# Performance work log

Measured on AMD Instinct MI355X. Metric: run time of the kernel, lower is better.

## Reference

```python
import math
import jax, jax.numpy as jnp
import numpy as np

_INIT_LOG_GAIN = math.log(5.0)
B, L, D = 4, 1024, 256


def setup_inputs() -> dict:
    key = jax.random.key(0)
    kq, kk = jax.random.split(key)
    q = jax.random.normal(kq, (B, L, D), dtype=jnp.float32)
    k = jax.random.normal(kk, (B, L, D), dtype=jnp.float32)
    P_prev = jnp.zeros((B, D, D), dtype=jnp.float32)
    log_gain = jnp.full((D,), _INIT_LOG_GAIN, dtype=jnp.float32)
    output_scale = jnp.ones((D,), dtype=jnp.float32)
    return {"q": q, "k": k, "P_prev": P_prev, "log_gain": log_gain,
            "output_scale": output_scale}


def reference(q, k, P_prev, log_gain, output_scale):
    """Sequential rank-1 projection-state update + normalized matvec + gated tanh.

    q, k: [B, L, D]; P_prev: [B, D, D]. Returns (q_out [B,L,D], P_final [B,D,D]).
    """
    gain = jnp.exp(log_gain)  # effective gain, [D]

    def step(P, qk_t):
        q_t, k_t = qk_t                                   # each [B, D]
        P = P + jnp.einsum('bi,bj->bij', k_t, k_t)        # rank-1 update
        fro = jnp.sqrt(jnp.sum(P * P, axis=(-2, -1), keepdims=True))
        P_norm = P / (fro + 1e-7)
        q_aligned = jnp.einsum('bij,bj->bi', P_norm, q_t)
        q_safe = jnp.tanh(gain * q_aligned) * output_scale
        return P, q_safe

    # scan over the L time axis
    P_final, outs = jax.lax.scan(step, P_prev,
                                 (jnp.swapaxes(q, 0, 1), jnp.swapaxes(k, 0, 1)))
    q_out = jnp.swapaxes(outs, 0, 1)  # [B, L, D]
    return q_out, P_final
```

## Files before the change

kernel.cpp:

```cpp
#include <hip/hip_runtime.h>
#include <math.h>


typedef __attribute__((ext_vector_type(8))) short bf16x8;
typedef __attribute__((ext_vector_type(4))) float f32x4;

__device__ __forceinline__ unsigned short f2bf(float x) {
    union { float f; unsigned u; } c; c.f = x;
    return (unsigned short)((c.u + (0x7fffu + ((c.u >> 16) & 1u))) >> 16);
}
__device__ __forceinline__ unsigned f2bf2(float a, float b) {
    union { float f; unsigned u; } ca, cb; ca.f = a; cb.f = b;
    unsigned ua = ca.u + (0x7fffu + ((ca.u >> 16) & 1u));
    unsigned ub = cb.u + (0x7fffu + ((cb.u >> 16) & 1u));
    return (ua >> 16) | (ub & 0xffff0000u);
}
__device__ __forceinline__ float bf2f(unsigned short h) {
    union { unsigned u; float f; } c; c.u = ((unsigned)h) << 16; return c.f;
}
__device__ __forceinline__ void gload16(const void* g, const void* l) {
    __builtin_amdgcn_global_load_lds(
        (const __attribute__((address_space(1))) unsigned int*)g,
        (__attribute__((address_space(3))) unsigned int*)l, 16, 0, 0);
}
__device__ __forceinline__ bf16x8 ldsfrag(const unsigned short* lds, int row0, int g0, int lane) {
    int r = row0 + (lane & 15);
    int g = g0 + (lane >> 4);
    return *(const bf16x8*)(lds + r * 64 + (((g ^ (r & 7)) & 7) << 3));
}
#define MFMA16(a, b, c) __builtin_amdgcn_mfma_f32_16x16x32_bf16(a, b, c, 0, 0, 0)

__global__ __launch_bounds__(256) void k_prep(
    const float* __restrict__ Q, const float* __restrict__ K,
    const float* __restrict__ Pprev,
    unsigned short* __restrict__ Qb, unsigned short* __restrict__ Kb,
    unsigned short* __restrict__ KThi, unsigned short* __restrict__ KTlo,
    float* __restrict__ basePart, int B_, int L, int D)
{
    __shared__ float lds[64 * 65];
    int tid = threadIdx.x, lane = tid & 63, w = tid >> 6;
    int nDt = D >> 6, nLt = L >> 6;
    int nC = B_ * nLt * nDt;
    int id = blockIdx.x;
    if (id < nC) {
        int dt = id % nDt, lt = (id / nDt) % nLt, b = id / (nDt * nLt);
        int l0 = lt * 64, d0 = dt * 64;
        const float* Qf = Q + (size_t)b * L * D;
        const float* Kf = K + (size_t)b * L * D;
        unsigned short* Qbp = Qb + (size_t)b * L * D;
        unsigned short* Kbp = Kb + (size_t)b * L * D;
        unsigned short* KThp = KThi + (size_t)b * D * L;
        unsigned short* KTlp = KTlo + (size_t)b * D * L;
        int r = tid >> 2, cq = (tid & 3) << 4;
#pragma unroll
        for (int i = 0; i < 16; i += 4) {
            float4 qv = *(const float4*)(Qf + (size_t)(l0 + r) * D + d0 + cq + i);
            float4 kv = *(const float4*)(Kf + (size_t)(l0 + r) * D + d0 + cq + i);
            uint2 qo; qo.x = f2bf2(qv.x, qv.y); qo.y = f2bf2(qv.z, qv.w);
            uint2 ko; ko.x = f2bf2(kv.x, kv.y); ko.y = f2bf2(kv.z, kv.w);
            *(uint2*)(Qbp + (size_t)(l0 + r) * D + d0 + cq + i) = qo;
            *(uint2*)(Kbp + (size_t)(l0 + r) * D + d0 + cq + i) = ko;
            lds[r * 65 + cq + i]     = kv.x; lds[r * 65 + cq + i + 1] = kv.y;
            lds[r * 65 + cq + i + 2] = kv.z; lds[r * 65 + cq + i + 3] = kv.w;
        }
        __syncthreads();
        int d2 = tid >> 2, cl = (tid & 3) << 4;
#pragma unroll
        for (int i = 0; i < 16; i += 2) {
            float v0 = lds[(cl + i) * 65 + d2];
            float v1 = lds[(cl + i + 1) * 65 + d2];
            unsigned short h0 = f2bf(v0), h1 = f2bf(v1);
            size_t off = (size_t)(d0 + d2) * L + l0 + cl + i;
            *(unsigned*)(KThp + off) = (unsigned)h0 | ((unsigned)h1 << 16);
            *(unsigned*)(KTlp + off) = f2bf2(v0 - bf2f(h0), v1 - bf2f(h1));
        }
    } else {
        int id2 = id - nC;
        int n = D * D / 16;
        const float* P = Pprev + (size_t)(id2 >> 4) * D * D + (size_t)(id2 & 15) * n;
        float s = 0.f;
        for (int i = tid * 4; i < n; i += 1024) {
            float4 vv = *(const float4*)(P + i);
            s += vv.x * vv.x + vv.y * vv.y + vv.z * vv.z + vv.w * vv.w;
        }
#pragma unroll
        for (int off = 32; off; off >>= 1) s += __shfl_down(s, off);
        if (lane == 0) lds[w] = s;
        __syncthreads();
        if (tid == 0) basePart[id2] = lds[0] + lds[1] + lds[2] + lds[3];
    }
}

__global__ __launch_bounds__(256) void k_gs(
    const unsigned short* __restrict__ Qb, const unsigned short* __restrict__ Kb,
    unsigned short* __restrict__ Sc, float* __restrict__ r2d,
    int B_, int L, int D, int nT, int nPairs)
{
    __shared__ unsigned short smem[24576];
    int tid = threadIdx.x, lane = tid & 63, w = tid >> 6;
    int fr = lane & 15, fq = lane >> 4;
    int nGS = B_ * nPairs;
    int bx = blockIdx.x;
    int id = (bx & 7) * (nGS >> 3) + (bx >> 3);

    int p = id % nPairs;
    int b = id / nPairs;
    int ti = (int)((sqrtf(8.f * p + 1.f) - 1.f) * 0.5f);
    while ((ti + 1) * (ti + 2) / 2 <= p) ti++;
    while (ti * (ti + 1) / 2 > p) ti--;
    int sj = p - ti * (ti + 1) / 2;

    const unsigned short* Qp = Qb + (size_t)b * L * D;
    const unsigned short* Kp = Kb + (size_t)b * L * D;
    int t0 = ti * 64, s0 = sj * 64;
    int wr = w >> 1, wc = w & 1;

    f32x4 g00 = {0,0,0,0}, g01 = {0,0,0,0}, g10 = {0,0,0,0}, g11 = {0,0,0,0};
    f32x4 s00 = {0,0,0,0}, s01 = {0,0,0,0}, s10 = {0,0,0,0}, s11 = {0,0,0,0};

    auto STAGE = [&](int ck, int bo) {
        const unsigned short* Kt = Kp + (size_t)t0 * D + ck * 64;
        const unsigned short* Qt = Qp + (size_t)t0 * D + ck * 64;
        const unsigned short* Ks = Kp + (size_t)s0 * D + ck * 64;
        for (int c = w; c < 8; c += 4) {
            int lrow = c * 8 + (lane >> 3);
            int gof = lrow * D + ((((lane & 7) ^ (lrow & 7)) & 7) << 3);
            gload16(Kt + gof, smem + bo + c * 512);
            gload16(Qt + gof, smem + bo + 4096 + c * 512);
            gload16(Ks + gof, smem + bo + 8192 + c * 512);
        }
    };

    STAGE(0, 0);
    __syncthreads();
    for (int ck = 0; ck < 4; ck++) {
        int cur = (ck & 1) * 12288;
        if (ck < 3) STAGE(ck + 1, 12288 - cur);
        const unsigned short* Kt = smem + cur;
        const unsigned short* Qt = Kt + 4096;
        const unsigned short* Ks = Kt + 8192;
#pragma unroll
        for (int kc = 0; kc < 2; kc++) {
            bf16x8 bK0 = ldsfrag(Ks, wc * 32, kc * 4, lane);
            bf16x8 bK1 = ldsfrag(Ks, wc * 32 + 16, kc * 4, lane);
            bf16x8 aK0 = ldsfrag(Kt, wr * 32, kc * 4, lane);
            bf16x8 aK1 = ldsfrag(Kt, wr * 32 + 16, kc * 4, lane);
            bf16x8 aQ0 = ldsfrag(Qt, wr * 32, kc * 4, lane);
            bf16x8 aQ1 = ldsfrag(Qt, wr * 32 + 16, kc * 4, lane);
            g00 = MFMA16(aK0, bK0, g00);
            g01 = MFMA16(aK0, bK1, g01);
            g10 = MFMA16(aK1, bK0, g10);
            g11 = MFMA16(aK1, bK1, g11);
            s00 = MFMA16(aQ0, bK0, s00);
            s01 = MFMA16(aQ0, bK1, s01);
            s10 = MFMA16(aQ1, bK0, s10);
            s11 = MFMA16(aQ1, bK1, s11);
        }
        __syncthreads();
    }

    float rsv[2][4] = {{0, 0, 0, 0}, {0, 0, 0, 0}};
#define EPI(MI, NI, AG, AS) { _Pragma("unroll") \
    for (int reg = 0; reg < 4; reg++) { \
        int tl = wr * 32 + MI * 16 + fq * 4 + reg; \
        int sl2 = wc * 32 + NI * 16 + fr; \
        int t = ti * 64 + tl, s = sj * 64 + sl2; \
        float g = AG[reg]; \
        float wgt = (s < t) ? 2.f : (s == t ? 1.f : 0.f); \
        rsv[MI][reg] += wgt * g * g; \
        smem[tl * 64 + sl2] = f2bf((s <= t) ? AS[reg] : 0.f); \
    } }
    EPI(0, 0, g00, s00) EPI(0, 1, g01, s01)
    EPI(1, 0, g10, s10) EPI(1, 1, g11, s11)
#undef EPI
    __syncthreads();
    {
        unsigned short* ScT = Sc + ((size_t)(b * nPairs + p) << 12);
        const uint4* s4 = (const uint4*)smem;
        uint4* d4 = (uint4*)ScT;
        d4[tid] = s4[tid];
        d4[tid + 256] = s4[tid + 256];
    }
#pragma unroll
    for (int off = 1; off < 16; off <<= 1) {
#pragma unroll
        for (int mi = 0; mi < 2; mi++)
#pragma unroll
            for (int reg = 0; reg < 4; reg++)
                rsv[mi][reg] += __shfl_xor(rsv[mi][reg], off);
    }
    if (fr == 0) {
#pragma unroll
        for (int mi = 0; mi < 2; mi++)
#pragma unroll
            for (int reg = 0; reg < 4; reg++) {
                int t = ti * 64 + wr * 32 + mi * 16 + fq * 4 + reg;
                r2d[((size_t)(b * 2 * nT) + sj * 2 + wc) * L + t] = rsv[mi][reg];
            }
    }
}

__global__ __launch_bounds__(256) void k_scan(
    const float* __restrict__ K, const float* __restrict__ Pprev,
    const float* __restrict__ r2d, const float* __restrict__ basePart,
    float* __restrict__ invfro, int B_, int L, int D, int nT)
{
    __shared__ float wred[4];
    int b = blockIdx.x;
    int tid = threadIdx.x, lane = tid & 63, w = tid >> 6;
    float bb = 0.f;
#pragma unroll
    for (int i = 0; i < 16; i++) bb += basePart[b * 16 + i];

    int t0v = tid * 4;
    int ns = 2 * ((t0v >> 6) + 1);
    float4 vs = {0.f, 0.f, 0.f, 0.f};
    for (int j = 0; j < ns; j++) {
        float4 rr = *(const float4*)&r2d[((size_t)(b * 2 * nT) + j) * L + t0v];
        vs.x += rr.x; vs.y += rr.y; vs.z += rr.z; vs.w += rr.w;
    }
    float v[4] = {vs.x, vs.y, vs.z, vs.w};
    if (bb != 0.f) {
#pragma unroll
        for (int u2 = 0; u2 < 4; u2++) {
            int t = t0v + u2;
            const float* kt = K + ((size_t)b * L + t) * D;
            const float* P = Pprev + (size_t)b * D * D;
            float c = 0.f;
            for (int i = 0; i < D; i++) {
                float a2 = 0.f;
                for (int j2 = 0; j2 < D; j2++) a2 += P[i * D + j2] * kt[j2];
                c += kt[i] * a2;
            }
            v[u2] += 2.f * c;
        }
    }
    v[1] += v[0]; v[2] += v[1]; v[3] += v[2];
    float tot = v[3], sc2 = tot;
    for (int off = 1; off < 64; off <<= 1) {
        float n2 = __shfl_up(sc2, off);
        if (lane >= off) sc2 += n2;
    }
    if (lane == 63) wred[w] = sc2;
    __syncthreads();
    float woff = 0.f;
    for (int i2 = 0; i2 < w; i2++) woff += wred[i2];
    float exc = woff + sc2 - tot;
#pragma unroll
    for (int u2 = 0; u2 < 4; u2++)
        invfro[(size_t)b * L + t0v + u2] = 1.f / (sqrtf(bb + exc + v[u2]) + 1e-7f);
}

__global__ __launch_bounds__(256) void k_yp(
    const float* __restrict__ Q,
    const float* __restrict__ Pprev, const float* __restrict__ log_gain,
    const float* __restrict__ oscale,
    const unsigned short* __restrict__ Sc, const float* __restrict__ invfro,
    const unsigned short* __restrict__ KThi, const unsigned short* __restrict__ KTlo,
    const float* __restrict__ basePart,
    float* __restrict__ out, float* __restrict__ outP,
    int B_, int L, int D, int nT, int nPairs)
{
    __shared__ unsigned short ys[18432];
    __shared__ float invf[1024];
    int tid = threadIdx.x, lane = tid & 63, w = tid >> 6;
    int fr = lane & 15, fq = lane >> 4;
    int nDt = D >> 6;
    int nDh = 16;
    int nP = B_ * nDt * nDt;
    int nY = B_ * (nT >> 1) * nDh;
    int bx = blockIdx.x;

    if (bx < nP) {
        int id2 = bx;
        int b = id2 >> 4, ij = id2 & 15;
        int i0 = (ij >> 2) << 6, j0 = (ij & 3) << 6;
        const unsigned short* Hb = KThi + (size_t)b * D * L;
        const unsigned short* Lb = KTlo + (size_t)b * D * L;
        int wr = w >> 1, wc = w & 1;
        unsigned short* Ah = ys;
        unsigned short* Al = ys + 4096;
        unsigned short* Bh = ys + 8192;
        unsigned short* Bl = ys + 12288;

        f32x4 c00 = {0,0,0,0}, c01 = {0,0,0,0}, c10 = {0,0,0,0}, c11 = {0,0,0,0};
        for (int ck = 0; ck < 16; ck++) {
            __syncthreads();
            for (int c = w; c < 8; c += 4) {
                int lrow = c * 8 + (lane >> 3);
                int gof = (((lane & 7) ^ (lrow & 7)) & 7) << 3;
                gload16(Hb + (size_t)(i0 + lrow) * L + ck * 64 + gof, Ah + c * 512);
                gload16(Lb + (size_t)(i0 + lrow) * L + ck * 64 + gof, Al + c * 512);
                gload16(Hb + (size_t)(j0 + lrow) * L + ck * 64 + gof, Bh + c * 512);
                gload16(Lb + (size_t)(j0 + lrow) * L + ck * 64 + gof, Bl + c * 512);
            }
            __syncthreads();
#pragma unroll
            for (int kc = 0; kc < 2; kc++) {
                bf16x8 ah0 = ldsfrag(Ah, wr * 32, kc * 4, lane);
                bf16x8 ah1 = ldsfrag(Ah, wr * 32 + 16, kc * 4, lane);
                bf16x8 al0 = ldsfrag(Al, wr * 32, kc * 4, lane);
                bf16x8 al1 = ldsfrag(Al, wr * 32 + 16, kc * 4, lane);
                bf16x8 bh0 = ldsfrag(Bh, wc * 32, kc * 4, lane);
                bf16x8 bh1 = ldsfrag(Bh, wc * 32 + 16, kc * 4, lane);
                bf16x8 bl0 = ldsfrag(Bl, wc * 32, kc * 4, lane);
                bf16x8 bl1 = ldsfrag(Bl, wc * 32 + 16, kc * 4, lane);
                c00 = MFMA16(ah0, bh0, c00); c00 = MFMA16(ah0, bl0, c00); c00 = MFMA16(al0, bh0, c00);
                c01 = MFMA16(ah0, bh1, c01); c01 = MFMA16(ah0, bl1, c01); c01 = MFMA16(al0, bh1, c01);
                c10 = MFMA16(ah1, bh0, c10); c10 = MFMA16(ah1, bl0, c10); c10 = MFMA16(al1, bh0, c10);
                c11 = MFMA16(ah1, bh1, c11); c11 = MFMA16(ah1, bl1, c11); c11 = MFMA16(al1, bh1, c11);
            }
        }
        const float* Pb = Pprev + (size_t)b * D * D;
        float* Ob = outP + (size_t)b * D * D;
#define PEPI(MI, NI, ACC) { _Pragma("unroll") \
        for (int reg = 0; reg < 4; reg++) { \
            int i = i0 + wr * 32 + MI * 16 + fq * 4 + reg; \
            int j = j0 + wc * 32 + NI * 16 + fr; \
            Ob[(size_t)i * D + j] = Pb[(size_t)i * D + j] + ACC[reg]; \
        } }
        PEPI(0, 0, c00) PEPI(0, 1, c01) PEPI(1, 0, c10) PEPI(1, 1, c11)
#undef PEPI
        return;
    }

    int yid = bx - nP;
    int id = (yid & 7) * (nY >> 3) + (yid >> 3);
    int dh = id % nDh;
    int u = (id / nDh) % (nT >> 1);
    int b = id / (nDh * (nT >> 1));
    int d0 = dh * 16;

    float bb = 0.f;
#pragma unroll
    for (int i = 0; i < 16; i++) bb += basePart[b * 16 + i];
    *(float4*)&invf[tid * 4] = *(const float4*)&invfro[(size_t)b * L + tid * 4];
    __syncthreads();

    int twl = w << 4;
    int ti0 = u, ti1 = nT - 1 - u;
    int pb0 = ti0 * (ti0 + 1) / 2, pb1 = ti1 * (ti1 + 1) / 2;
    const unsigned short* ScB = Sc + ((size_t)b * nPairs << 12);
    const unsigned short* KTb = KThi + (size_t)b * D * L;

    f32x4 c0 = {0, 0, 0, 0};
    f32x4 c1 = {0, 0, 0, 0};

    auto STAGE = [&](int sj, int bo) {
        const unsigned short* T1p = ScB + ((size_t)(pb1 + sj) << 12);
        if (sj <= u) {
            const unsigned short* T0p = ScB + ((size_t)(pb0 + sj) << 12);
            for (int c = w; c < 8; c += 4) {
                int lrow = c * 8 + (lane >> 3);
                int go = lrow * 64 + ((((lane & 7) ^ (lrow & 7)) & 7) << 3);
                gload16(T0p + go, ys + bo + c * 512);
            }
        }
        for (int c = w; c < 8; c += 4) {
            int lrow = c * 8 + (lane >> 3);
            int go = lrow * 64 + ((((lane & 7) ^ (lrow & 7)) & 7) << 3);
            gload16(T1p + go, ys + bo + 4096 + c * 512);
        }
        if (w < 2) {
            int lrow = w * 8 + (lane >> 3);
            int gsw = (((lane & 7) ^ (lrow & 7)) & 7) << 3;
            gload16(KTb + (size_t)(d0 + lrow) * L + sj * 64 + gsw,
                    ys + bo + 8192 + w * 512);
        }
    };

    STAGE(0, 0);
    __syncthreads();
    for (int sj = 0; sj <= ti1; sj++) {
        int cur = (sj & 1) * 9216;
        if (sj < ti1) STAGE(sj + 1, 9216 - cur);
        const unsigned short* S0 = ys + cur;
        const unsigned short* S1 = S0 + 4096;
        const unsigned short* KTl = S0 + 8192;
#pragma unroll
        for (int kc = 0; kc < 2; kc++) {
            bf16x8 b0 = ldsfrag(KTl, 0, kc * 4, lane);
            bf16x8 A1 = ldsfrag(S1, twl, kc * 4, lane);
            c1 = MFMA16(A1, b0, c1);
            if (sj <= ti0) {
                bf16x8 A0 = ldsfrag(S0, twl, kc * 4, lane);
                c0 = MFMA16(A0, b0, c0);
            }
        }
        __syncthreads();
    }

    if (bb != 0.f) {
        const float* Qf = Q + (size_t)b * L * D;
        const float* Pb = Pprev + (size_t)b * D * D;
        for (int jj = 0; jj < D; jj++) {
            float p0 = Pb[(size_t)(d0 + fr) * D + jj];
#pragma unroll
            for (int reg = 0; reg < 4; reg++) {
                float q0v = Qf[(size_t)(ti0 * 64 + twl + fq * 4 + reg) * D + jj];
                float q1v = Qf[(size_t)(ti1 * 64 + twl + fq * 4 + reg) * D + jj];
                c0[reg] += q0v * p0;
                c1[reg] += q1v * p0;
            }
        }
    }

    float gg0 = expf(log_gain[d0 + fr]), os0 = oscale[d0 + fr];
    float* outb = out + (size_t)b * L * D;
#pragma unroll
    for (int reg = 0; reg < 4; reg++) {
        int t0 = ti0 * 64 + twl + fq * 4 + reg;
        int t1 = ti1 * 64 + twl + fq * 4 + reg;
        outb[(size_t)t0 * D + d0 + fr] = tanhf(gg0 * c0[reg] * invf[t0]) * os0;
        outb[(size_t)t1 * D + d0 + fr] = tanhf(gg0 * c1[reg] * invf[t1]) * os0;
    }
}

extern "C" void kernel_launch(void* const* d_in, const int* in_sizes, int n_in,
                              void* d_out, int out_size, void* d_ws, size_t ws_size,
                              hipStream_t stream) {
    const float* q = (const float*)d_in[0];
    const float* k = (const float*)d_in[1];
    const float* Pprev = (const float*)d_in[2];
    const float* log_gain = (const float*)d_in[3];
    const float* oscale = (const float*)d_in[4];

    int D = in_sizes[3];
    int B = in_sizes[2] / (D * D);
    int L = in_sizes[0] / (B * D);
    int nT = L / 64;
    int nPairs = nT * (nT + 1) / 2;
    int nDt = D >> 6;
    int nLt = L >> 6;

    if (D != 256 || L != 1024) return;

    float* out = (float*)d_out;
    float* outP = out + (size_t)B * L * D;

    size_t sR = (size_t)B * L * 2 * nT;
    size_t sBP = 64;
    size_t sI = (size_t)B * L;
    size_t sSc = (size_t)B * nPairs * 4096;
    size_t sLD = (size_t)B * L * D;
    size_t sKT = (size_t)B * D * L;
    size_t need = (sR + sBP + sI) * sizeof(float) + (sSc + 2 * sLD + 2 * sKT) * 2;
    if (ws_size < need) return;

    float* r2d = (float*)d_ws;
    float* basePart = r2d + sR;
    float* invfro = basePart + sBP;
    unsigned short* Sc = (unsigned short*)(invfro + sI);
    unsigned short* Qb = Sc + sSc;
    unsigned short* Kb = Qb + sLD;
    unsigned short* KThi = Kb + sLD;
    unsigned short* KTlo = KThi + sKT;

    int grid0 = B * nLt * nDt + B * 16;
    int grid1 = B * nPairs;
    int grid2 = B * nDt * nDt + B * (nT >> 1) * 16;

    k_prep<<<grid0, 256, 0, stream>>>(q, k, Pprev, Qb, Kb, KThi, KTlo, basePart, B, L, D);
    k_gs<<<grid1, 256, 0, stream>>>(Qb, Kb, Sc, r2d, B, L, D, nT, nPairs);
    k_scan<<<B, 256, 0, stream>>>(k, Pprev, r2d, basePart, invfro, B, L, D, nT);
    k_yp<<<grid2, 256, 0, stream>>>(q, Pprev, log_gain, oscale, Sc, invfro, KThi, KTlo,
                                    basePart, out, outP, B, L, D, nT, nPairs);
}
```

Measured before the change: 48.96 us.

## Split Y accumulation across two blocks by K parity and reduce in new kernel

Each Y task in k_yp now runs as two blocks that take alternating sj chunks, doubling the number of Y blocks so more CUs are in use and each block's serial loop is shorter. Each block writes its partial 128x16 result as bf16 to a workspace buffer. A new k_red kernel sums the two partials and applies the Pprev correction, the Frobenius normalisation, the gain, tanh and the output scale. This costs an extra launch, extra global traffic for the partials, and bf16 rounding of the partial sums before the epilogue.

After: 53.73 us. 1.1x slower.

```diff
diff --git a/kernel.cpp b/kernel.cpp
--- a/kernel.cpp
+++ b/kernel.cpp
@@ -17,6 +17,12 @@
 }
 __device__ __forceinline__ float bf2f(unsigned short h) {
     union { unsigned u; float f; } c; c.u = ((unsigned)h) << 16; return c.f;
+}
+__device__ __forceinline__ float bflo(unsigned u) {
+    union { unsigned u; float f; } c; c.u = u << 16; return c.f;
+}
+__device__ __forceinline__ float bfhi(unsigned u) {
+    union { unsigned u; float f; } c; c.u = u & 0xffff0000u; return c.f;
 }
 __device__ __forceinline__ void gload16(const void* g, const void* l) {
     __builtin_amdgcn_global_load_lds(
@@ -252,23 +258,19 @@
 }
 
 __global__ __launch_bounds__(256) void k_yp(
-    const float* __restrict__ Q,
-    const float* __restrict__ Pprev, const float* __restrict__ log_gain,
-    const float* __restrict__ oscale,
-    const unsigned short* __restrict__ Sc, const float* __restrict__ invfro,
+    const float* __restrict__ Pprev,
+    const unsigned short* __restrict__ Sc,
     const unsigned short* __restrict__ KThi, const unsigned short* __restrict__ KTlo,
-    const float* __restrict__ basePart,
-    float* __restrict__ out, float* __restrict__ outP,
+    unsigned short* __restrict__ Ypart, float* __restrict__ outP,
     int B_, int L, int D, int nT, int nPairs)
 {
     __shared__ unsigned short ys[18432];
-    __shared__ float invf[1024];
     int tid = threadIdx.x, lane = tid & 63, w = tid >> 6;
     int fr = lane & 15, fq = lane >> 4;
     int nDt = D >> 6;
     int nDh = 16;
     int nP = B_ * nDt * nDt;
-    int nY = B_ * (nT >> 1) * nDh;
+    int nY = B_ * (nT >> 1) * nDh * 2;
     int bx = blockIdx.x;
 
     if (bx < nP) {
@@ -326,16 +328,12 @@
 
     int yid = bx - nP;
     int id = (yid & 7) * (nY >> 3) + (yid >> 3);
-    int dh = id % nDh;
-    int u = (id / nDh) % (nT >> 1);
-    int b = id / (nDh * (nT >> 1));
+    int c = id & 1;
+    int rest = id >> 1;
+    int dh = rest % nDh;
+    int u = (rest / nDh) % (nT >> 1);
+    int b = rest / (nDh * (nT >> 1));
     int d0 = dh * 16;
-
-    float bb = 0.f;
-#pragma unroll
-    for (int i = 0; i < 16; i++) bb += basePart[b * 16 + i];
-    *(float4*)&invf[tid * 4] = *(const float4*)&invfro[(size_t)b * L + tid * 4];
-    __syncthreads();
 
     int twl = w << 4;
     int ti0 = u, ti1 = nT - 1 - u;
@@ -350,16 +348,16 @@
         const unsigned short* T1p = ScB + ((size_t)(pb1 + sj) << 12);
         if (sj <= u) {
             const unsigned short* T0p = ScB + ((size_t)(pb0 + sj) << 12);
-            for (int c = w; c < 8; c += 4) {
-                int lrow = c * 8 + (lane >> 3);
+            for (int cc = w; cc < 8; cc += 4) {
+                int lrow = cc * 8 + (lane >> 3);
                 int go = lrow * 64 + ((((lane & 7) ^ (lrow & 7)) & 7) << 3);
-                gload16(T0p + go, ys + bo + c * 512);
+                gload16(T0p + go, ys + bo + cc * 512);
             }
         }
-        for (int c = w; c < 8; c += 4) {
-            int lrow = c * 8 + (lane >> 3);
+        for (int cc = w; cc < 8; cc += 4) {
+            int lrow = cc * 8 + (lane >> 3);
             int go = lrow * 64 + ((((lane & 7) ^ (lrow & 7)) & 7) << 3);
-            gload16(T1p + go, ys + bo + 4096 + c * 512);
+            gload16(T1p + go, ys + bo + 4096 + cc * 512);
         }
         if (w < 2) {
             int lrow = w * 8 + (lane >> 3);
@@ -369,11 +367,12 @@
         }
     };
 
-    STAGE(0, 0);
+    STAGE(c, 0);
     __syncthreads();
-    for (int sj = 0; sj <= ti1; sj++) {
-        int cur = (sj & 1) * 9216;
-        if (sj < ti1) STAGE(sj + 1, 9216 - cur);
+    for (int sj = c; sj <= ti1; sj += 2) {
+        int it = (sj - c) >> 1;
+        int cur = (it & 1) * 9216;
+        if (sj + 2 <= ti1) STAGE(sj + 2, 9216 - cur);
         const unsigned short* S0 = ys + cur;
         const unsigned short* S1 = S0 + 4096;
         const unsigned short* KTl = S0 + 8192;
@@ -390,30 +389,63 @@
         __syncthreads();
     }
 
+    unsigned short* yp = Ypart + ((size_t)id << 11);
+#pragma unroll
+    for (int reg = 0; reg < 4; reg++) {
+        int r0 = twl + fq * 4 + reg;
+        yp[r0 * 16 + fr] = f2bf(c0[reg]);
+        yp[(64 + r0) * 16 + fr] = f2bf(c1[reg]);
+    }
+}
+
+__global__ __launch_bounds__(256) void k_red(
+    const unsigned short* __restrict__ Ypart, const float* __restrict__ invfro,
+    const float* __restrict__ log_gain, const float* __restrict__ oscale,
+    const float* __restrict__ Q, const float* __restrict__ Pprev,
+    const float* __restrict__ basePart,
+    float* __restrict__ out, int B_, int L, int D, int nT)
+{
+    size_t e = ((size_t)blockIdx.x * 256 + threadIdx.x) * 8;
+    int b = (int)(e / ((size_t)L * D));
+    int rem = (int)(e % ((size_t)L * D));
+    int t = rem / D, d = rem % D;
+    int ti = t >> 6;
+    int u = ti < (nT >> 1) ? ti : (nT - 1 - ti);
+    int row = (ti >= (nT >> 1) ? 64 : 0) + (t & 63);
+    int dh = d >> 4;
+    int task = ((b * (nT >> 1) + u) * 16 + dh) << 1;
+    const unsigned short* p0 = Ypart + ((size_t)task << 11) + row * 16 + (d & 15);
+    const unsigned short* p1 = p0 + 2048;
+    uint4 a = *(const uint4*)p0;
+    uint4 q2 = *(const uint4*)p1;
+    float s[8];
+    s[0] = bflo(a.x) + bflo(q2.x); s[1] = bfhi(a.x) + bfhi(q2.x);
+    s[2] = bflo(a.y) + bflo(q2.y); s[3] = bfhi(a.y) + bfhi(q2.y);
+    s[4] = bflo(a.z) + bflo(q2.z); s[5] = bfhi(a.z) + bfhi(q2.z);
+    s[6] = bflo(a.w) + bflo(q2.w); s[7] = bfhi(a.w) + bfhi(q2.w);
+
+    float bb = 0.f;
+#pragma unroll
+    for (int i = 0; i < 16; i++) bb += basePart[b * 16 + i];
     if (bb != 0.f) {
-        const float* Qf = Q + (size_t)b * L * D;
+        const float* Qt = Q + ((size_t)b * L + t) * D;
         const float* Pb = Pprev + (size_t)b * D * D;
         for (int jj = 0; jj < D; jj++) {
-            float p0 = Pb[(size_t)(d0 + fr) * D + jj];
-#pragma unroll
-            for (int reg = 0; reg < 4; reg++) {
-                float q0v = Qf[(size_t)(ti0 * 64 + twl + fq * 4 + reg) * D + jj];
-                float q1v = Qf[(size_t)(ti1 * 64 + twl + fq * 4 + reg) * D + jj];
-                c0[reg] += q0v * p0;
-                c1[reg] += q1v * p0;
-            }
-        }
-    }
-
-    float gg0 = expf(log_gain[d0 + fr]), os0 = oscale[d0 + fr];
-    float* outb = out + (size_t)b * L * D;
-#pragma unroll
-    for (int reg = 0; reg < 4; reg++) {
-        int t0 = ti0 * 64 + twl + fq * 4 + reg;
-        int t1 = ti1 * 64 + twl + fq * 4 + reg;
-        outb[(size_t)t0 * D + d0 + fr] = tanhf(gg0 * c0[reg] * invf[t0]) * os0;
-        outb[(size_t)t1 * D + d0 + fr] = tanhf(gg0 * c1[reg] * invf[t1]) * os0;
-    }
+            float qv = Qt[jj];
+#pragma unroll
+            for (int j = 0; j < 8; j++) s[j] += qv * Pb[(size_t)(d + j) * D + jj];
+        }
+    }
+
+    float inv = invfro[(size_t)b * L + t];
+    float o[8];
+#pragma unroll
+    for (int j = 0; j < 8; j++)
+        o[j] = tanhf(expf(log_gain[d + j]) * s[j] * inv) * oscale[d + j];
+    float4 o0 = {o[0], o[1], o[2], o[3]};
+    float4 o1 = {o[4], o[5], o[6], o[7]};
+    *(float4*)(out + e) = o0;
+    *(float4*)(out + e + 4) = o1;
 }
 
 extern "C" void kernel_launch(void* const* d_in, const int* in_sizes, int n_in,
@@ -444,7 +476,8 @@
     size_t sSc = (size_t)B * nPairs * 4096;
     size_t sLD = (size_t)B * L * D;
     size_t sKT = (size_t)B * D * L;
-    size_t need = (sR + sBP + sI) * sizeof(float) + (sSc + 2 * sLD + 2 * sKT) * 2;
+    size_t sYp = (size_t)B * (nT >> 1) * 16 * 2 * 2048;
+    size_t need = (sR + sBP + sI) * sizeof(float) + (sSc + 2 * sLD + 2 * sKT + sYp) * 2;
     if (ws_size < need) return;
 
     float* r2d = (float*)d_ws;
@@ -455,14 +488,18 @@
     unsigned short* Kb = Qb + sLD;
     unsigned short* KThi = Kb + sLD;
     unsigned short* KTlo = KThi + sKT;
+    unsigned short* Ypart = KTlo + sKT;
 
     int grid0 = B * nLt * nDt + B * 16;
     int grid1 = B * nPairs;
-    int grid2 = B * nDt * nDt + B * (nT >> 1) * 16;
+    int grid2 = B * nDt * nDt + B * (nT >> 1) * 16 * 2;
+    int grid3 = (int)(((size_t)B * L * D / 8 + 255) / 256);
 
     k_prep<<<grid0, 256, 0, stream>>>(q, k, Pprev, Qb, Kb, KThi, KTlo, basePart, B, L, D);
     k_gs<<<grid1, 256, 0, stream>>>(Qb, Kb, Sc, r2d, B, L, D, nT, nPairs);
     k_scan<<<B, 256, 0, stream>>>(k, Pprev, r2d, basePart, invfro, B, L, D, nT);
-    k_yp<<<grid2, 256, 0, stream>>>(q, Pprev, log_gain, oscale, Sc, invfro, KThi, KTlo,
-                                    basePart, out, outP, B, L, D, nT, nPairs);
-}
+    k_yp<<<grid2, 256, 0, stream>>>(Pprev, Sc, KThi, KTlo, Ypart, outP,
+                                    B, L, D, nT, nPairs);
+    k_red<<<grid3, 256, 0, stream>>>(Ypart, invfro, log_gain, oscale, q, Pprev,
+                                     basePart, out, B, L, D, nT);
+}
```
